# Optimization experiments

Hardware: AMD Instinct MI355X
Metric: run time of the kernel (lower is better)

Reference implementation:

```python
import jax, jax.numpy as jnp
import numpy as np

EMBED = 1024
HEADS = 16
HEAD_DIM = EMBED // HEADS
BATCH = 2
SEQ = 256

def setup_inputs() -> dict:
    key = jax.random.key(0)
    ks = jax.random.split(key, 6)
    x = jax.random.normal(ks[0], (BATCH, SEQ, EMBED), dtype=jnp.float32)
    s = 1.0 / np.sqrt(HEAD_DIM)
    Wq = jax.random.uniform(ks[1], (HEAD_DIM, HEAD_DIM), jnp.float32, -s, s)
    Wk = jax.random.uniform(ks[2], (HEAD_DIM, HEAD_DIM), jnp.float32, -s, s)
    Wv = jax.random.uniform(ks[3], (HEAD_DIM, HEAD_DIM), jnp.float32, -s, s)
    so = 1.0 / np.sqrt(EMBED)
    Wo = jax.random.uniform(ks[4], (EMBED, EMBED), jnp.float32, -so, so)
    bo = jax.random.uniform(ks[5], (EMBED,), jnp.float32, -so, so)
    return {"x": x, "Wq": Wq, "Wk": Wk, "Wv": Wv, "Wo": Wo, "bo": bo}

def reference(x, Wq, Wk, Wv, Wo, bo):
    n, s, e = x.shape
    xr = x.reshape(n, s, HEADS, HEAD_DIM)          # (n,s,h,d)
    # nn.Linear applies x @ W.T
    q = jnp.einsum('nshd,ed->nshe', xr, Wq)
    k = jnp.einsum('nshd,ed->nshe', xr, Wk)
    v = jnp.einsum('nshd,ed->nshe', xr, Wv)
    # elementwise outer-product score: (n,s,t,h,d), no reduction over d
    energy = q[:, :, None, :, :] * k[:, None, :, :, :]
    # NOTE: original code softmaxes over dim=3 == the HEADS axis
    attn = jax.nn.softmax(energy / jnp.float32(np.sqrt(EMBED)), axis=3)
    out = jnp.einsum('nsthd,nthd->nshd', attn, v)  # reduce over t
    out = out.reshape(n, s, HEADS * HEAD_DIM)
    return out @ Wo.T + bo
```

## Files before the change

### kernel.cpp

```cpp
#include <hip/hip_runtime.h>

#define NB 2
#define SQL 256
#define NH 16
#define HD 64
#define EMB 1024

typedef unsigned short ushortT;
typedef unsigned int uintT;
typedef __attribute__((ext_vector_type(8))) short bf16x8;
typedef __attribute__((ext_vector_type(4))) float f32x4;
typedef __attribute__((ext_vector_type(2))) float f32x2;

__device__ __constant__ float kQSCALE = 1.4426950408889634f / 32.0f;

__device__ __forceinline__ float fexp2(float x) { return __builtin_amdgcn_exp2f(x); }
__device__ __forceinline__ float frcp(float x)  { return __builtin_amdgcn_rcpf(x); }

__device__ __forceinline__ ushortT f2bf(float x) {
    uintT u = __float_as_uint(x);
    u += 0x7fffu + ((u >> 16) & 1u);
    return (ushortT)(u >> 16);
}
__device__ __forceinline__ ushort4 f2bf4(float4 a) {
    return make_ushort4(f2bf(a.x), f2bf(a.y), f2bf(a.z), f2bf(a.w));
}
__device__ __forceinline__ f32x2 unpk2(uintT u) {
    f32x2 r;
    r.x = __uint_as_float(u << 16);
    r.y = __uint_as_float(u & 0xffff0000u);
    return r;
}
__device__ __forceinline__ float pairsum_dpp(float u) {
    const int j = __builtin_amdgcn_mov_dpp(__float_as_int(u), 0xB1, 0xF, 0xF, true);
    return u + __int_as_float(j);
}

__global__ __launch_bounds__(256) void qkv_kernel(
    const float* __restrict__ x,
    const float* __restrict__ Wq,
    const float* __restrict__ Wk,
    const float* __restrict__ Wv,
    const float* __restrict__ Wo,
    const float* __restrict__ bo,
    ushortT* __restrict__ Q,
    ushortT* __restrict__ K,
    ushortT* __restrict__ V,
    float* __restrict__ AO,
    float* __restrict__ out,
    ushortT* __restrict__ Wob)
{
    __shared__ ushortT wls[3][64 * 72];
    __shared__ ushortT xs[2][16 * 72];

    const int tid = threadIdx.x;
    const int ns0 = blockIdx.x * 2;
    const int g   = blockIdx.x * 256 + tid;

    {
        const float4 z = make_float4(0.f, 0.f, 0.f, 0.f);
        ((float4*)AO)[g] = z;
        ((float4*)AO)[g + 65536] = z;
        const float4 bb = ((const float4*)bo)[g & 255];
        ((float4*)out)[g] = bb;
        ((float4*)out)[g + 65536] = bb;
    }
#pragma unroll
    for (int j = 0; j < 4; ++j) {
        const int f4 = j * 65536 + g;
        ((ushort4*)Wob)[f4] = f2bf4(((const float4*)Wo)[f4]);
    }

#pragma unroll
    for (int m = 0; m < 3; ++m) {
        const float4* src = (m == 0) ? (const float4*)Wq
                          : (m == 1) ? (const float4*)Wk : (const float4*)Wv;
#pragma unroll
        for (int j = 0; j < 4; ++j) {
            const int idx = j * 256 + tid;
            const int e   = idx >> 4;
            const int d4  = idx & 15;
            float4 a = src[idx];
            if (m == 0) { a.x *= kQSCALE; a.y *= kQSCALE; a.z *= kQSCALE; a.w *= kQSCALE; }
            *(ushort4*)&wls[m][e * 72 + d4 * 4] = f2bf4(a);
        }
    }
#pragma unroll
    for (int j = 0; j < 2; ++j) {
        const int idx = j * 256 + tid;
        const int r   = idx >> 8;
        const int h   = (idx >> 4) & 15;
        const int d4  = idx & 15;
        const float4 a = ((const float4*)(x + (size_t)(ns0 + r) * EMB))[idx & 255];
        *(ushort4*)&xs[r][h * 72 + d4 * 4] = f2bf4(a);
    }
    __syncthreads();

    const int w   = tid >> 6;
    const int nsr = w >> 1;
    const int eb0 = (w & 1) * 32;
    const int l   = tid & 63;
    const int lr  = l & 15;
    const int lk  = l >> 4;

    const bf16x8 a0 = *(const bf16x8*)&xs[nsr][lr * 72 + lk * 8];
    const bf16x8 a1 = *(const bf16x8*)&xs[nsr][lr * 72 + 32 + lk * 8];

#pragma unroll
    for (int m = 0; m < 3; ++m) {
        ushortT* outp = (m == 0) ? Q : (m == 1) ? K : V;
#pragma unroll
        for (int ef = 0; ef < 2; ++ef) {
            const int eb = eb0 + ef * 16;
            const bf16x8 b0 = *(const bf16x8*)&wls[m][(eb + lr) * 72 + lk * 8];
            const bf16x8 b1 = *(const bf16x8*)&wls[m][(eb + lr) * 72 + 32 + lk * 8];
            f32x4 c = {0.f, 0.f, 0.f, 0.f};
            c = __builtin_amdgcn_mfma_f32_16x16x32_bf16(a0, b0, c, 0, 0, 0);
            c = __builtin_amdgcn_mfma_f32_16x16x32_bf16(a1, b1, c, 0, 0, 0);
            ushortT* dst = outp + (size_t)(ns0 + nsr) * EMB + (eb + lr) * 16 + lk * 4;
            *(ushort4*)dst = make_ushort4(f2bf(c[0]), f2bf(c[1]), f2bf(c[2]), f2bf(c[3]));
        }
    }
}

#define ATTN_STEP(KU4, VU4)                                                    \
    {                                                                          \
        f32x2 k2[4], v2[4], p0[4], p1[4];                                      \
        k2[0] = unpk2(KU4.x); k2[1] = unpk2(KU4.y);                            \
        k2[2] = unpk2(KU4.z); k2[3] = unpk2(KU4.w);                            \
        _Pragma("unroll")                                                      \
        for (int j = 0; j < 4; ++j) {                                          \
            const f32x2 x0 = q0_2[j] * k2[j];                                  \
            const f32x2 x1 = q1_2[j] * k2[j];                                  \
            p0[j].x = fexp2(x0.x); p0[j].y = fexp2(x0.y);                      \
            p1[j].x = fexp2(x1.x); p1[j].y = fexp2(x1.y);                      \
        }                                                                      \
        const f32x2 s0v = (p0[0] + p0[1]) + (p0[2] + p0[3]);                   \
        const f32x2 s1v = (p1[0] + p1[1]) + (p1[2] + p1[3]);                   \
        const float rs0 = frcp(pairsum_dpp(s0v.x + s0v.y));                    \
        const float rs1 = frcp(pairsum_dpp(s1v.x + s1v.y));                    \
        const f32x2 rb0 = {rs0, rs0};                                          \
        const f32x2 rb1 = {rs1, rs1};                                          \
        v2[0] = unpk2(VU4.x); v2[1] = unpk2(VU4.y);                            \
        v2[2] = unpk2(VU4.z); v2[3] = unpk2(VU4.w);                            \
        _Pragma("unroll")                                                      \
        for (int j = 0; j < 4; ++j) {                                          \
            acc0[j] = __builtin_elementwise_fma(v2[j] * rb0, p0[j], acc0[j]);  \
            acc1[j] = __builtin_elementwise_fma(v2[j] * rb1, p1[j], acc1[j]);  \
        }                                                                      \
    }

__global__ __launch_bounds__(256) void attn_kernel(
    const ushortT* __restrict__ Q,
    const ushortT* __restrict__ K,
    const ushortT* __restrict__ V,
    float* __restrict__ AO)
{
    __shared__ float red[16][256];

    const int b    = blockIdx.x;
    const int tw   = b & 1;
    const int eh   = (b >> 1) & 1;
    const int sg   = (b >> 2) & 127;
    const int n    = b >> 9;
    const int wave = threadIdx.x >> 6;
    const int l    = threadIdx.x & 63;
    const int s0   = sg * 2;
    const int t0   = tw * 128 + wave * 32;

    f32x2 q0_2[4], q1_2[4];
    {
        const uint4* qp = (const uint4*)(Q + (size_t)(n * SQL + s0) * EMB + 512 * eh) + l;
        const uint4 qa = qp[0];
        const uint4 qb = qp[128];
        q0_2[0] = unpk2(qa.x); q0_2[1] = unpk2(qa.y);
        q0_2[2] = unpk2(qa.z); q0_2[3] = unpk2(qa.w);
        q1_2[0] = unpk2(qb.x); q1_2[1] = unpk2(qb.y);
        q1_2[2] = unpk2(qb.z); q1_2[3] = unpk2(qb.w);
    }

    f32x2 acc0[4], acc1[4];
#pragma unroll
    for (int j = 0; j < 4; ++j) {
        acc0[j] = (f32x2){0.f, 0.f};
        acc1[j] = (f32x2){0.f, 0.f};
    }

    const uint4* kp = (const uint4*)(K + (size_t)(n * SQL + t0) * EMB + 512 * eh) + l;
    const uint4* vp = (const uint4*)(V + (size_t)(n * SQL + t0) * EMB + 512 * eh) + l;

    uint4 ka = kp[0];
    uint4 kb = kp[128];
    uint4 va = vp[0];

#pragma unroll
    for (int tt = 0; tt < 32; tt += 2) {
        const uint4 kn2 = kp[256];
        const uint4 vb  = vp[128];
        ATTN_STEP(ka, va);
        const uint4 kn3 = kp[384];
        va = vp[256];
        kp += 256; vp += 256;
        ATTN_STEP(kb, vb);
        ka = kn2; kb = kn3;
    }

#pragma unroll
    for (int j = 0; j < 4; ++j) {
        red[2 * j    ][wave * 64 + l] = acc0[j].x;
        red[2 * j + 1][wave * 64 + l] = acc0[j].y;
        red[8 + 2 * j    ][wave * 64 + l] = acc1[j].x;
        red[8 + 2 * j + 1][wave * 64 + l] = acc1[j].y;
    }
    __syncthreads();

    float* aob = AO + (size_t)(n * SQL + s0) * EMB + 512 * (l & 1) + 32 * eh + (l >> 1);
#pragma unroll
    for (int di = 0; di < 4; ++di) {
        const int i = wave * 4 + di;
        const float sum = (red[i][l] + red[i][64 + l]) + (red[i][128 + l] + red[i][192 + l]);
        const int s = i >> 3;
        const int c = i & 7;
        atomicAdd(aob + (size_t)s * EMB + 64 * c, sum);
    }
}

__global__ __launch_bounds__(512) void proj_kernel(
    const float* __restrict__ AO,
    const ushortT* __restrict__ Wob,
    float* __restrict__ out)
{
    __shared__ ushortT As[64 * 40];
    __shared__ ushortT Bs[128 * 40];

    const int b  = blockIdx.x;
    const int kc = b & 3;
    const int jt = (b >> 2) & 7;
    const int rt = b >> 5;
    const int tid = threadIdx.x;
    const int r0 = rt * 64, j0 = jt * 128, k0 = kc * 256;

    const int w  = tid >> 6;
    const int wr = w >> 2;
    const int wc = w & 3;
    const int l  = tid & 63;
    const int lr = l & 15;
    const int lk = l >> 4;

    f32x4 c00 = {0.f, 0.f, 0.f, 0.f};
    f32x4 c01 = {0.f, 0.f, 0.f, 0.f};
    f32x4 c10 = {0.f, 0.f, 0.f, 0.f};
    f32x4 c11 = {0.f, 0.f, 0.f, 0.f};

    for (int kt = 0; kt < 8; ++kt) {
        const int kb = k0 + kt * 32;
        __syncthreads();
        {
            const int row = tid >> 3;
            const int kq  = tid & 7;
            const float4 a = *(const float4*)&AO[(size_t)(r0 + row) * EMB + kb + kq * 4];
            *(ushort4*)&As[row * 40 + kq * 4] = f2bf4(a);
        }
        {
            const int row = tid >> 2;
            const int ko  = tid & 3;
            const uint4 wv = *(const uint4*)&Wob[(size_t)(j0 + row) * EMB + kb + ko * 8];
            *(uint4*)&Bs[row * 40 + ko * 8] = wv;
        }
        __syncthreads();

        const bf16x8 a0 = *(const bf16x8*)&As[(wr * 32 + lr) * 40 + lk * 8];
        const bf16x8 a1 = *(const bf16x8*)&As[(wr * 32 + 16 + lr) * 40 + lk * 8];
        const bf16x8 b0 = *(const bf16x8*)&Bs[(wc * 32 + lr) * 40 + lk * 8];
        const bf16x8 b1 = *(const bf16x8*)&Bs[(wc * 32 + 16 + lr) * 40 + lk * 8];
        c00 = __builtin_amdgcn_mfma_f32_16x16x32_bf16(a0, b0, c00, 0, 0, 0);
        c01 = __builtin_amdgcn_mfma_f32_16x16x32_bf16(a0, b1, c01, 0, 0, 0);
        c10 = __builtin_amdgcn_mfma_f32_16x16x32_bf16(a1, b0, c10, 0, 0, 0);
        c11 = __builtin_amdgcn_mfma_f32_16x16x32_bf16(a1, b1, c11, 0, 0, 0);
    }

    const int rbase = r0 + wr * 32 + lk * 4;
    const int jbase = j0 + wc * 32 + lr;
#pragma unroll
    for (int e = 0; e < 4; ++e) {
        atomicAdd(&out[(size_t)(rbase + e) * EMB + jbase],           c00[e]);
        atomicAdd(&out[(size_t)(rbase + e) * EMB + jbase + 16],      c01[e]);
        atomicAdd(&out[(size_t)(rbase + 16 + e) * EMB + jbase],      c10[e]);
        atomicAdd(&out[(size_t)(rbase + 16 + e) * EMB + jbase + 16], c11[e]);
    }
}

extern "C" void kernel_launch(void* const* d_in, const int* in_sizes, int n_in,
                              void* d_out, int out_size, void* d_ws, size_t ws_size,
                              hipStream_t stream)
{
    const float* x  = (const float*)d_in[0];
    const float* Wq = (const float*)d_in[1];
    const float* Wk = (const float*)d_in[2];
    const float* Wv = (const float*)d_in[3];
    const float* Wo = (const float*)d_in[4];
    const float* bo = (const float*)d_in[5];

    float* ws = (float*)d_ws;
    ushortT* Q   = (ushortT*)ws;
    ushortT* K   = (ushortT*)(ws + 262144);
    ushortT* V   = (ushortT*)(ws + 524288);
    float*   AO  = ws + 786432;
    ushortT* Wob = (ushortT*)(ws + 1310720);

    qkv_kernel<<<256, 256, 0, stream>>>(x, Wq, Wk, Wv, Wo, bo, Q, K, V, AO,
                                        (float*)d_out, Wob);
    attn_kernel<<<1024, 256, 0, stream>>>(Q, K, V, AO);
    proj_kernel<<<256, 512, 0, stream>>>(AO, Wob, (float*)d_out);
}
```

Before: 50.04 us.

## Remove atomics: full-T reduction per attn block and unsplit-K projection with bias

Result: slower. 71.25 us (+42.4%).

```diff
diff --git a/kernel.cpp b/kernel.cpp
--- a/kernel.cpp
+++ b/kernel.cpp
@@ -42,12 +42,9 @@
     const float* __restrict__ Wk,
     const float* __restrict__ Wv,
     const float* __restrict__ Wo,
-    const float* __restrict__ bo,
     ushortT* __restrict__ Q,
     ushortT* __restrict__ K,
     ushortT* __restrict__ V,
-    float* __restrict__ AO,
-    float* __restrict__ out,
     ushortT* __restrict__ Wob)
 {
     __shared__ ushortT wls[3][64 * 72];
@@ -57,14 +54,6 @@
     const int ns0 = blockIdx.x * 2;
     const int g   = blockIdx.x * 256 + tid;
 
-    {
-        const float4 z = make_float4(0.f, 0.f, 0.f, 0.f);
-        ((float4*)AO)[g] = z;
-        ((float4*)AO)[g + 65536] = z;
-        const float4 bb = ((const float4*)bo)[g & 255];
-        ((float4*)out)[g] = bb;
-        ((float4*)out)[g + 65536] = bb;
-    }
 #pragma unroll
     for (int j = 0; j < 4; ++j) {
         const int f4 = j * 65536 + g;
@@ -150,23 +139,23 @@
         }                                                                      \
     }
 
-__global__ __launch_bounds__(256) void attn_kernel(
+__global__ __launch_bounds__(512) void attn_kernel(
     const ushortT* __restrict__ Q,
     const ushortT* __restrict__ K,
     const ushortT* __restrict__ V,
     float* __restrict__ AO)
 {
-    __shared__ float red[16][256];
+    __shared__ float red[16][512];
 
     const int b    = blockIdx.x;
-    const int tw   = b & 1;
-    const int eh   = (b >> 1) & 1;
-    const int sg   = (b >> 2) & 127;
-    const int n    = b >> 9;
-    const int wave = threadIdx.x >> 6;
-    const int l    = threadIdx.x & 63;
+    const int eh   = b & 1;
+    const int sg   = (b >> 1) & 127;
+    const int n    = b >> 8;
+    const int tid  = threadIdx.x;
+    const int wave = tid >> 6;
+    const int l    = tid & 63;
     const int s0   = sg * 2;
-    const int t0   = tw * 128 + wave * 32;
+    const int t0   = wave * 32;
 
     f32x2 q0_2[4], q1_2[4];
     {
@@ -194,7 +183,7 @@
     uint4 va = vp[0];
 
 #pragma unroll
-    for (int tt = 0; tt < 32; tt += 2) {
+    for (int tt = 0; tt < 30; tt += 2) {
         const uint4 kn2 = kp[256];
         const uint4 vb  = vp[128];
         ATTN_STEP(ka, va);
@@ -204,45 +193,52 @@
         ATTN_STEP(kb, vb);
         ka = kn2; kb = kn3;
     }
+    {
+        const uint4 vb = vp[128];
+        ATTN_STEP(ka, va);
+        ATTN_STEP(kb, vb);
+    }
 
 #pragma unroll
     for (int j = 0; j < 4; ++j) {
-        red[2 * j    ][wave * 64 + l] = acc0[j].x;
-        red[2 * j + 1][wave * 64 + l] = acc0[j].y;
-        red[8 + 2 * j    ][wave * 64 + l] = acc1[j].x;
-        red[8 + 2 * j + 1][wave * 64 + l] = acc1[j].y;
+        red[2 * j        ][tid] = acc0[j].x;
+        red[2 * j + 1    ][tid] = acc0[j].y;
+        red[8 + 2 * j    ][tid] = acc1[j].x;
+        red[8 + 2 * j + 1][tid] = acc1[j].y;
     }
     __syncthreads();
 
     float* aob = AO + (size_t)(n * SQL + s0) * EMB + 512 * (l & 1) + 32 * eh + (l >> 1);
 #pragma unroll
-    for (int di = 0; di < 4; ++di) {
-        const int i = wave * 4 + di;
-        const float sum = (red[i][l] + red[i][64 + l]) + (red[i][128 + l] + red[i][192 + l]);
+    for (int di = 0; di < 2; ++di) {
+        const int i = wave * 2 + di;
+        float sum = 0.f;
+#pragma unroll
+        for (int ww = 0; ww < 8; ++ww) sum += red[i][ww * 64 + l];
         const int s = i >> 3;
         const int c = i & 7;
-        atomicAdd(aob + (size_t)s * EMB + 64 * c, sum);
-    }
-}
-
-__global__ __launch_bounds__(512) void proj_kernel(
+        aob[(size_t)s * EMB + 64 * c] = sum;
+    }
+}
+
+__global__ __launch_bounds__(256) void proj_kernel(
     const float* __restrict__ AO,
     const ushortT* __restrict__ Wob,
+    const float* __restrict__ bo,
     float* __restrict__ out)
 {
     __shared__ ushortT As[64 * 40];
-    __shared__ ushortT Bs[128 * 40];
+    __shared__ ushortT Bs[64 * 40];
 
     const int b  = blockIdx.x;
-    const int kc = b & 3;
-    const int jt = (b >> 2) & 7;
-    const int rt = b >> 5;
+    const int jt = b & 15;
+    const int rt = b >> 4;
     const int tid = threadIdx.x;
-    const int r0 = rt * 64, j0 = jt * 128, k0 = kc * 256;
+    const int r0 = rt * 64, j0 = jt * 64;
 
     const int w  = tid >> 6;
-    const int wr = w >> 2;
-    const int wc = w & 3;
+    const int wr = w >> 1;
+    const int wc = w & 1;
     const int l  = tid & 63;
     const int lr = l & 15;
     const int lk = l >> 4;
@@ -252,12 +248,14 @@
     f32x4 c10 = {0.f, 0.f, 0.f, 0.f};
     f32x4 c11 = {0.f, 0.f, 0.f, 0.f};
 
-    for (int kt = 0; kt < 8; ++kt) {
-        const int kb = k0 + kt * 32;
+    for (int kt = 0; kt < 32; ++kt) {
+        const int kb = kt * 32;
         __syncthreads();
-        {
-            const int row = tid >> 3;
-            const int kq  = tid & 7;
+#pragma unroll
+        for (int it = 0; it < 2; ++it) {
+            const int f   = it * 256 + tid;
+            const int row = f >> 3;
+            const int kq  = f & 7;
             const float4 a = *(const float4*)&AO[(size_t)(r0 + row) * EMB + kb + kq * 4];
             *(ushort4*)&As[row * 40 + kq * 4] = f2bf4(a);
         }
@@ -281,12 +279,14 @@
 
     const int rbase = r0 + wr * 32 + lk * 4;
     const int jbase = j0 + wc * 32 + lr;
+    const float bb0 = bo[jbase];
+    const float bb1 = bo[jbase + 16];
 #pragma unroll
     for (int e = 0; e < 4; ++e) {
-        atomicAdd(&out[(size_t)(rbase + e) * EMB + jbase],           c00[e]);
-        atomicAdd(&out[(size_t)(rbase + e) * EMB + jbase + 16],      c01[e]);
-        atomicAdd(&out[(size_t)(rbase + 16 + e) * EMB + jbase],      c10[e]);
-        atomicAdd(&out[(size_t)(rbase + 16 + e) * EMB + jbase + 16], c11[e]);
+        out[(size_t)(rbase + e) * EMB + jbase]           = c00[e] + bb0;
+        out[(size_t)(rbase + e) * EMB + jbase + 16]      = c01[e] + bb1;
+        out[(size_t)(rbase + 16 + e) * EMB + jbase]      = c10[e] + bb0;
+        out[(size_t)(rbase + 16 + e) * EMB + jbase + 16] = c11[e] + bb1;
     }
 }
 
@@ -308,8 +308,7 @@
     float*   AO  = ws + 786432;
     ushortT* Wob = (ushortT*)(ws + 1310720);
 
-    qkv_kernel<<<256, 256, 0, stream>>>(x, Wq, Wk, Wv, Wo, bo, Q, K, V, AO,
-                                        (float*)d_out, Wob);
-    attn_kernel<<<1024, 256, 0, stream>>>(Q, K, V, AO);
-    proj_kernel<<<256, 512, 0, stream>>>(AO, Wob, (float*)d_out);
-}
+    qkv_kernel<<<256, 256, 0, stream>>>(x, Wq, Wk, Wv, Wo, Q, K, V, Wob);
+    attn_kernel<<<512, 512, 0, stream>>>(Q, K, V, AO);
+    proj_kernel<<<128, 256, 0, stream>>>(AO, Wob, bo, (float*)d_out);
+}
```

## Drop split-K atomics in output projection, fuse bias, prefetch tiles

Applied to the files above, without the earlier changes.

Measured after the change: 50.26 us. Within noise of the previous version (+0.4%).

```diff
diff --git a/kernel.cpp b/kernel.cpp
--- a/kernel.cpp
+++ b/kernel.cpp
@@ -42,12 +42,10 @@
     const float* __restrict__ Wk,
     const float* __restrict__ Wv,
     const float* __restrict__ Wo,
-    const float* __restrict__ bo,
     ushortT* __restrict__ Q,
     ushortT* __restrict__ K,
     ushortT* __restrict__ V,
     float* __restrict__ AO,
-    float* __restrict__ out,
     ushortT* __restrict__ Wob)
 {
     __shared__ ushortT wls[3][64 * 72];
@@ -61,9 +59,6 @@
         const float4 z = make_float4(0.f, 0.f, 0.f, 0.f);
         ((float4*)AO)[g] = z;
         ((float4*)AO)[g + 65536] = z;
-        const float4 bb = ((const float4*)bo)[g & 255];
-        ((float4*)out)[g] = bb;
-        ((float4*)out)[g + 65536] = bb;
     }
 #pragma unroll
     for (int j = 0; j < 4; ++j) {
@@ -194,7 +189,7 @@
     uint4 va = vp[0];
 
 #pragma unroll
-    for (int tt = 0; tt < 32; tt += 2) {
+    for (int tt = 0; tt < 30; tt += 2) {
         const uint4 kn2 = kp[256];
         const uint4 vb  = vp[128];
         ATTN_STEP(ka, va);
@@ -204,11 +199,16 @@
         ATTN_STEP(kb, vb);
         ka = kn2; kb = kn3;
     }
+    {
+        const uint4 vb = vp[128];
+        ATTN_STEP(ka, va);
+        ATTN_STEP(kb, vb);
+    }
 
 #pragma unroll
     for (int j = 0; j < 4; ++j) {
-        red[2 * j    ][wave * 64 + l] = acc0[j].x;
-        red[2 * j + 1][wave * 64 + l] = acc0[j].y;
+        red[2 * j        ][wave * 64 + l] = acc0[j].x;
+        red[2 * j + 1    ][wave * 64 + l] = acc0[j].y;
         red[8 + 2 * j    ][wave * 64 + l] = acc1[j].x;
         red[8 + 2 * j + 1][wave * 64 + l] = acc1[j].y;
     }
@@ -225,68 +225,63 @@
     }
 }
 
-__global__ __launch_bounds__(512) void proj_kernel(
+__global__ __launch_bounds__(256) void proj_kernel(
     const float* __restrict__ AO,
     const ushortT* __restrict__ Wob,
+    const float* __restrict__ bo,
     float* __restrict__ out)
 {
-    __shared__ ushortT As[64 * 40];
-    __shared__ ushortT Bs[128 * 40];
+    __shared__ ushortT As[32 * 40];
+    __shared__ ushortT Bs[64 * 40];
 
     const int b  = blockIdx.x;
-    const int kc = b & 3;
-    const int jt = (b >> 2) & 7;
-    const int rt = b >> 5;
+    const int jt = b & 15;
+    const int rt = b >> 4;
     const int tid = threadIdx.x;
-    const int r0 = rt * 64, j0 = jt * 128, k0 = kc * 256;
+    const int r0 = rt * 32, j0 = jt * 64;
 
     const int w  = tid >> 6;
-    const int wr = w >> 2;
-    const int wc = w & 3;
+    const int wr = w >> 1;
+    const int wc = w & 1;
     const int l  = tid & 63;
     const int lr = l & 15;
     const int lk = l >> 4;
 
-    f32x4 c00 = {0.f, 0.f, 0.f, 0.f};
-    f32x4 c01 = {0.f, 0.f, 0.f, 0.f};
-    f32x4 c10 = {0.f, 0.f, 0.f, 0.f};
-    f32x4 c11 = {0.f, 0.f, 0.f, 0.f};
-
-    for (int kt = 0; kt < 8; ++kt) {
-        const int kb = k0 + kt * 32;
+    const int arow = tid >> 3, akq = tid & 7;
+    const int brow = tid >> 2, bko = tid & 3;
+
+    f32x4 c0 = {0.f, 0.f, 0.f, 0.f};
+    f32x4 c1 = {0.f, 0.f, 0.f, 0.f};
+
+    float4 aN = *(const float4*)&AO[(size_t)(r0 + arow) * EMB + akq * 4];
+    uint4  bN = *(const uint4*)&Wob[(size_t)(j0 + brow) * EMB + bko * 8];
+
+    for (int kt = 0; kt < 32; ++kt) {
         __syncthreads();
-        {
-            const int row = tid >> 3;
-            const int kq  = tid & 7;
-            const float4 a = *(const float4*)&AO[(size_t)(r0 + row) * EMB + kb + kq * 4];
-            *(ushort4*)&As[row * 40 + kq * 4] = f2bf4(a);
-        }
-        {
-            const int row = tid >> 2;
-            const int ko  = tid & 3;
-            const uint4 wv = *(const uint4*)&Wob[(size_t)(j0 + row) * EMB + kb + ko * 8];
-            *(uint4*)&Bs[row * 40 + ko * 8] = wv;
+        *(ushort4*)&As[arow * 40 + akq * 4] = f2bf4(aN);
+        *(uint4*)&Bs[brow * 40 + bko * 8] = bN;
+        if (kt < 31) {
+            const int kb = (kt + 1) * 32;
+            aN = *(const float4*)&AO[(size_t)(r0 + arow) * EMB + kb + akq * 4];
+            bN = *(const uint4*)&Wob[(size_t)(j0 + brow) * EMB + kb + bko * 8];
         }
         __syncthreads();
 
-        const bf16x8 a0 = *(const bf16x8*)&As[(wr * 32 + lr) * 40 + lk * 8];
-        const bf16x8 a1 = *(const bf16x8*)&As[(wr * 32 + 16 + lr) * 40 + lk * 8];
+        const bf16x8 a  = *(const bf16x8*)&As[(wr * 16 + lr) * 40 + lk * 8];
         const bf16x8 b0 = *(const bf16x8*)&Bs[(wc * 32 + lr) * 40 + lk * 8];
         const bf16x8 b1 = *(const bf16x8*)&Bs[(wc * 32 + 16 + lr) * 40 + lk * 8];
-        c00 = __builtin_amdgcn_mfma_f32_16x16x32_bf16(a0, b0, c00, 0, 0, 0);
-        c01 = __builtin_amdgcn_mfma_f32_16x16x32_bf16(a0, b1, c01, 0, 0, 0);
-        c10 = __builtin_amdgcn_mfma_f32_16x16x32_bf16(a1, b0, c10, 0, 0, 0);
-        c11 = __builtin_amdgcn_mfma_f32_16x16x32_bf16(a1, b1, c11, 0, 0, 0);
-    }
-
-    const int rbase = r0 + wr * 32 + lk * 4;
+        c0 = __builtin_amdgcn_mfma_f32_16x16x32_bf16(a, b0, c0, 0, 0, 0);
+        c1 = __builtin_amdgcn_mfma_f32_16x16x32_bf16(a, b1, c1, 0, 0, 0);
+    }
+
+    const int rbase = r0 + wr * 16 + lk * 4;
     const int jbase = j0 + wc * 32 + lr;
+    const float bb0 = bo[jbase];
+    const float bb1 = bo[jbase + 16];
 #pragma unroll
     for (int e = 0; e < 4; ++e) {
-        atomicAdd(&out[(size_t)(rbase + e) * EMB + jbase],           c00[e]);
-        atomicAdd(&out[(size_t)(rbase + e) * EMB + jbase + 16],      c01[e]);
-        atomicAdd(&out[(size_t)(rbase + 16 + e) * EMB + jbase],      c10[e]);
-        atomicAdd(&out[(size_t)(rbase + 16 + e) * EMB + jbase + 16], c11[e]);
+        out[(size_t)(rbase + e) * EMB + jbase]      = c0[e] + bb0;
+        out[(size_t)(rbase + e) * EMB + jbase + 16] = c1[e] + bb1;
     }
 }
 
@@ -308,8 +303,7 @@
     float*   AO  = ws + 786432;
     ushortT* Wob = (ushortT*)(ws + 1310720);
 
-    qkv_kernel<<<256, 256, 0, stream>>>(x, Wq, Wk, Wv, Wo, bo, Q, K, V, AO,
-                                        (float*)d_out, Wob);
+    qkv_kernel<<<256, 256, 0, stream>>>(x, Wq, Wk, Wv, Wo, Q, K, V, AO, Wob);
     attn_kernel<<<1024, 256, 0, stream>>>(Q, K, V, AO);
-    proj_kernel<<<256, 512, 0, stream>>>(AO, Wob, (float*)d_out);
-}
+    proj_kernel<<<256, 256, 0, stream>>>(AO, Wob, bo, (float*)d_out);
+}
```
